# Kernel optimization log

Measured on AMD Instinct MI355X. Metric: run time of the kernel, lower is better.

Reference implementation:

```python
import jax, jax.numpy as jnp
import numpy as np

N, L, E_Q, E_TOTAL, H, FORECAST = 4, 2048, 512, 512, 8, 8
E_HEAD = E_TOTAL // H
DT = 1.0
NEG = -1e30


def setup_inputs() -> dict:
    rng = jax.random.key(0)
    ks = jax.random.split(rng, 8)
    inv = 1.0 / np.sqrt(E_Q)
    return {
        "query": jax.random.normal(ks[0], (N, L, E_Q), jnp.float32),
        "key": jax.random.normal(ks[1], (N, L, E_Q), jnp.float32),
        "value": jax.random.normal(ks[2], (N, L, E_Q), jnp.float32),
        "Wqkv": jax.random.normal(ks[3], (E_Q, 3 * E_TOTAL), jnp.float32) * inv,
        "bqkv": jnp.zeros((3 * E_TOTAL,), jnp.float32),
        "Wo": jax.random.normal(ks[4], (E_TOTAL, E_Q), jnp.float32) * (1.0 / np.sqrt(E_TOTAL)),
        "bo": jnp.zeros((E_Q,), jnp.float32),
        "Xi": jax.random.normal(ks[5], (H, E_HEAD, E_HEAD), jnp.float32) * 0.02,
    }


def reference(query, key, value, Wqkv, bqkv, Wo, bo, Xi):
    # NOTE: original forward projects `query` into q,k,v (key/value args unused).
    b, s, _ = query.shape
    qkv = query @ Wqkv + bqkv                      # [b, s, 3E]
    q, k, v = jnp.split(qkv, 3, axis=-1)
    split_heads = lambda t: t.reshape(b, s, H, E_HEAD).transpose(0, 2, 1, 3)  # [b,H,s,h]
    q, k, v = split_heads(q), split_heads(k), split_heads(v)
    # causal SDPA
    scale = 1.0 / np.sqrt(E_HEAD)
    scores = jnp.einsum('bhqd,bhkd->bhqk', q, k) * scale
    causal = jnp.tril(jnp.ones((s, s), bool))
    scores = jnp.where(causal, scores, NEG)
    probs = jax.nn.softmax(scores, axis=-1)
    attn = jnp.einsum('bhqk,bhkd->bhqd', probs, v)  # [b,H,s,h]
    # per-head SINDy linear dynamics, strict symmetry -> skew-symmetric A
    A = Xi - jnp.swapaxes(Xi, -1, -2)               # [H,h,h]

    def step(x, _):
        x2 = x + DT * jnp.einsum('bhsd,hde->bhse', x, A)
        return x2, x2

    _, ys = jax.lax.scan(step, attn, None, length=FORECAST)  # [n,b,H,s,h]
    roll = jnp.transpose(ys, (1, 0, 3, 2, 4)).reshape(b, FORECAST, s, E_TOTAL)
    return roll @ Wo + bo                            # [b, n, s, E_q]
```

## Files before the change

### kernel.cpp

```cpp
#include <hip/hip_runtime.h>
#include <math.h>


#define NEGV -1e30f

typedef __bf16 bf16_t;
typedef __bf16 bf16x4 __attribute__((ext_vector_type(4)));
typedef __bf16 bf16x8 __attribute__((ext_vector_type(8)));
typedef float f32x4 __attribute__((ext_vector_type(4)));

#define MFMA(a, b, c) __builtin_amdgcn_mfma_f32_16x16x32_bf16((a), (b), (c), 0, 0, 0)

#define QSCALE 0.18033688011112042f

__device__ __forceinline__ bf16x8* swz_ptr(bf16_t* base, int r, int cb) {
  return (bf16x8*)((char*)base + r * 128 + (cb ^ ((r & 7) << 4)));
}
__device__ __forceinline__ const bf16x8* swz_cptr(const bf16_t* base, int r, int cb) {
  return (const bf16x8*)((const char*)base + r * 128 + (cb ^ ((r & 7) << 4)));
}

__device__ __forceinline__ void gload16(const bf16_t* g, bf16_t* l) {
  __builtin_amdgcn_global_load_lds(
      (const __attribute__((address_space(1))) void*)g,
      (__attribute__((address_space(3))) void*)l, 16, 0, 0);
}


__global__ __launch_bounds__(256) void xconv(const float* __restrict__ X,
                                             bf16_t* __restrict__ Xb) {
  const int gid = blockIdx.x * 256 + threadIdx.x;
  const int s = gid >> 6, j = gid & 63;
  const float4* src = (const float4*)(X + (size_t)s * 512 + j * 8);
  const float4 f0 = src[0], f1 = src[1];
  bf16x8 v;
  v[0] = (bf16_t)f0.x; v[1] = (bf16_t)f0.y; v[2] = (bf16_t)f0.z; v[3] = (bf16_t)f0.w;
  v[4] = (bf16_t)f1.x; v[5] = (bf16_t)f1.y; v[6] = (bf16_t)f1.z; v[7] = (bf16_t)f1.w;
  *(bf16x8*)&Xb[(size_t)s * 512 + (j >> 3) * 64 + 8 * ((j & 7) ^ (s & 7))] = v;
}

__global__ __launch_bounds__(256) void wconv(const float* __restrict__ W,
                                             bf16_t* __restrict__ WT) {
  const int n0 = blockIdx.x * 64, k0 = blockIdx.y * 64;
  __shared__ float Wf[64][65];
  const int tid = threadIdx.x;
#pragma unroll
  for (int c = 0; c < 16; ++c) {
    const int idx = tid + c * 256;
    const int kk = idx >> 6, nn = idx & 63;
    Wf[kk][nn] = W[(size_t)(k0 + kk) * 1536 + n0 + nn];
  }
  __syncthreads();
  const int nr = tid >> 2;
  const int jb = (tid & 3) * 2;
#pragma unroll
  for (int t = 0; t < 2; ++t) {
    const int j = jb + t;
    bf16x8 v;
#pragma unroll
    for (int i = 0; i < 8; ++i) v[i] = (bf16_t)Wf[j * 8 + i][nr];
    *(bf16x8*)&WT[(size_t)(n0 + nr) * 512 + k0 + 8 * (j ^ (nr & 7))] = v;
  }
}

__global__ __launch_bounds__(256) void build_powers(const float* __restrict__ Xi,
                                                    float* __restrict__ pows) {
  const int h = blockIdx.x;
  __shared__ __align__(16) float P[64][68];
  __shared__ __align__(16) float cur[64][68];
  const int tid = threadIdx.x;
  const float* xi = Xi + (size_t)h * 4096;
  float* dst = pows + (size_t)h * 8 * 4096;
  for (int idx = tid; idx < 4096; idx += 256) {
    const int i = idx >> 6, j = idx & 63;
    const float p = (i == j ? 1.f : 0.f) + xi[i * 64 + j] - xi[j * 64 + i];
    P[i][j] = p;
    cur[i][j] = p;
    dst[idx] = p;
  }
  __syncthreads();
  const int i = tid >> 2;
  const int j0 = (tid & 3) * 16;
  for (int n = 1; n < 8; ++n) {
    float a[16];
#pragma unroll
    for (int jj = 0; jj < 16; ++jj) a[jj] = 0.f;
    for (int dd = 0; dd < 64; ++dd) {
      const float c = cur[i][dd];
#pragma unroll
      for (int jj = 0; jj < 16; ++jj) a[jj] += c * P[dd][j0 + jj];
    }
    __syncthreads();
#pragma unroll
    for (int jj = 0; jj < 16; ++jj) {
      cur[i][j0 + jj] = a[jj];
      dst[n * 4096 + i * 64 + j0 + jj] = a[jj];
    }
    __syncthreads();
  }
}

__global__ __launch_bounds__(256) void build_B(const float* __restrict__ pows,
                                               const float* __restrict__ Wo,
                                               bf16_t* __restrict__ BmatT) {
  const int et = blockIdx.x;
  const int n = blockIdx.y;
  const int h = blockIdx.z;
  __shared__ __align__(16) float P[64][68];
  __shared__ __align__(16) float We[64][128];
  const int tid = threadIdx.x;
  const float* src = pows + ((size_t)h * 8 + n) * 4096;
  for (int idx = tid; idx < 4096; idx += 256) P[idx >> 6][idx & 63] = src[idx];
  const int e0 = et * 128;
  for (int idx = tid; idx < 8192; idx += 256) {
    const int dd = idx >> 7, e = idx & 127;
    We[dd][e] = Wo[(size_t)(h * 64 + dd) * 512 + e0 + e];
  }
  __syncthreads();
  const int d = tid >> 2;
  const int eq = (tid & 3) * 32;
  float acc[32];
#pragma unroll
  for (int j = 0; j < 32; ++j) acc[j] = 0.f;
  for (int dd = 0; dd < 64; ++dd) {
    const float p = P[d][dd];
#pragma unroll
    for (int j = 0; j < 32; ++j) acc[j] += p * We[dd][eq + j];
  }
  bf16_t* dst = BmatT + (size_t)n * 512 * 512 + (size_t)(e0 + eq) * 512 + h * 64;
  const int dlo = d & 7, dhi = d >> 3;
#pragma unroll
  for (int j = 0; j < 32; ++j)
    dst[(size_t)j * 512 + 8 * (dhi ^ (j & 7)) + dlo] = (bf16_t)acc[j];
}

__global__ __launch_bounds__(256) void qkv_gemm(const bf16_t* __restrict__ Xb,
                                                const bf16_t* __restrict__ WT,
                                                const float* __restrict__ bias,
                                                bf16_t* __restrict__ qw,
                                                bf16_t* __restrict__ kw,
                                                bf16_t* __restrict__ vt) {
  __shared__ __align__(16) bf16_t As[128 * 64];
  __shared__ __align__(16) bf16_t Bs[128 * 64];
  const int tid = threadIdx.x;
  const int wave = tid >> 6, lane = tid & 63;
  const int g = lane >> 4, li = lane & 15;
  const int row0 = blockIdx.x * 128;
  const int col0 = blockIdx.y * 128;
  const int wm = (wave >> 1) * 64, wn = (wave & 1) * 64;
  f32x4 acc[4][4] = {};
  const bf16_t* asrc = Xb + (size_t)(row0 + wave * 32 + (lane >> 3)) * 512 + (lane & 7) * 8;
  const bf16_t* bsrc = WT + (size_t)(col0 + wave * 32 + (lane >> 3)) * 512 + (lane & 7) * 8;
  bf16_t* adst = &As[wave * 32 * 64];
  bf16_t* bdst = &Bs[wave * 32 * 64];
  for (int k0 = 0; k0 < 512; k0 += 64) {
#pragma unroll
    for (int c = 0; c < 4; ++c) {
      gload16(asrc + (size_t)c * 8 * 512 + k0, adst + c * 512);
      gload16(bsrc + (size_t)c * 8 * 512 + k0, bdst + c * 512);
    }
    __syncthreads();
#pragma unroll
    for (int ks = 0; ks < 2; ++ks) {
      bf16x8 af[4], bfr[4];
#pragma unroll
      for (int mr = 0; mr < 4; ++mr)
        af[mr] = *swz_cptr(As, wm + mr * 16 + li, ks * 64 + g * 16);
#pragma unroll
      for (int nr = 0; nr < 4; ++nr)
        bfr[nr] = *swz_cptr(Bs, wn + nr * 16 + li, ks * 64 + g * 16);
#pragma unroll
      for (int mr = 0; mr < 4; ++mr)
#pragma unroll
        for (int nr = 0; nr < 4; ++nr)
          acc[mr][nr] = MFMA(af[mr], bfr[nr], acc[mr][nr]);
    }
    __syncthreads();
  }
  const int cbase = col0 + wn;
  const int sel = cbase >> 9;
  const int hh = (cbase & 511) >> 6;
  const int bb = row0 >> 11;
  const size_t hb = (size_t)(bb * 8 + hh) * (2048 * 64);
  if (sel == 2) {
    bf16_t* vbase = vt + hb;
#pragma unroll
    for (int nr = 0; nr < 4; ++nr) {
      const int dcol = nr * 16 + li;
      const float bv = bias[cbase + dcol];
#pragma unroll
      for (int mr = 0; mr < 4; ++mr) {
        bf16x4 pk;
#pragma unroll
        for (int i = 0; i < 4; ++i) pk[i] = (bf16_t)(acc[mr][nr][i] + bv);
        const int s = (row0 + wm + mr * 16 + g * 4) & 2047;
        *(bf16x4*)&vbase[(size_t)dcol * 2048 + s] = pk;
      }
    }
  } else {
    bf16_t* dstp = (sel == 0 ? qw : kw) + hb;
    const float sc = (sel == 0) ? QSCALE : 1.0f;
#pragma unroll
    for (int nr = 0; nr < 4; ++nr) {
      const int dcol = nr * 16 + li;
      const float bv = bias[cbase + dcol];
#pragma unroll
      for (int mr = 0; mr < 4; ++mr) {
#pragma unroll
        for (int i = 0; i < 4; ++i) {
          const int r = row0 + wm + mr * 16 + g * 4 + i;
          const int s = r & 2047;
          dstp[(size_t)s * 64 + dcol] = (bf16_t)((acc[mr][nr][i] + bv) * sc);
        }
      }
    }
  }
}

__global__ __launch_bounds__(256, 4) void fattn(const bf16_t* __restrict__ qw,
                                                const bf16_t* __restrict__ kw,
                                                const bf16_t* __restrict__ vt,
                                                bf16_t* __restrict__ attn) {
  __shared__ __align__(16) bf16_t Ks[2][64][64];
  __shared__ __align__(16) bf16_t Vs[2][64][64];
  __shared__ __align__(16) bf16_t Ps[4][16][64];
  const int tid = threadIdx.x;
  const int w = tid >> 6;
  const int lane = tid & 63;
  const int g = lane >> 4;
  const int li = lane & 15;
  const int qt = (int)gridDim.x - 1 - (int)blockIdx.x;
  const int h = blockIdx.y;
  const int b = blockIdx.z;
  const size_t base = ((size_t)(b * 8 + h)) * (2048 * 64);
  const int q0 = qt * 64;
  const int qrow = q0 + w * 16 + li;
  const bf16x8 aq0 = *(const bf16x8*)(qw + base + (size_t)qrow * 64 + g * 8);
  const bf16x8 aq1 = *(const bf16x8*)(qw + base + (size_t)qrow * 64 + 32 + g * 8);
  const bf16_t* kbase = kw + base;
  const bf16_t* vbase = vt + base;
  const int r_st = tid >> 2;
  const int qu = tid & 3;
  {
    const bf16_t* kp = kbase + (size_t)r_st * 64 + qu * 16;
    const bf16_t* vp = vbase + (size_t)r_st * 2048 + qu * 16;
    *swz_ptr(&Ks[0][0][0], r_st, qu * 32) = *(const bf16x8*)kp;
    *swz_ptr(&Ks[0][0][0], r_st, qu * 32 + 16) = *(const bf16x8*)(kp + 8);
    *swz_ptr(&Vs[0][0][0], r_st, qu * 32) = *(const bf16x8*)vp;
    *swz_ptr(&Vs[0][0][0], r_st, qu * 32 + 16) = *(const bf16x8*)(vp + 8);
  }
  f32x4 accO[4] = {};
  float m_run = -__builtin_inff();
  float l_run = 0.f;
  char* const psrow = (char*)&Ps[w][li][0];
  const int pswz = (li & 7) << 4;
  for (int kt = 0; kt <= qt; ++kt) {
    __syncthreads();
    const int cur = kt & 1;
    const bool pf = kt < qt;
    bf16x8 nk0, nk1, nv0, nv1;
    if (pf) {
      const int kb2 = (kt + 1) * 64;
      const bf16_t* kp = kbase + (size_t)(kb2 + r_st) * 64 + qu * 16;
      const bf16_t* vp = vbase + (size_t)r_st * 2048 + kb2 + qu * 16;
      nk0 = *(const bf16x8*)kp;
      nk1 = *(const bf16x8*)(kp + 8);
      nv0 = *(const bf16x8*)vp;
      nv1 = *(const bf16x8*)(vp + 8);
    }
    f32x4 sv[4];
    __builtin_amdgcn_s_setprio(1);
#pragma unroll
    for (int nt = 0; nt < 4; ++nt) {
      const bf16x8 bk0 = *swz_cptr(&Ks[cur][0][0], nt * 16 + li, g * 16);
      const bf16x8 bk1 = *swz_cptr(&Ks[cur][0][0], nt * 16 + li, 64 + g * 16);
      f32x4 z = {0.f, 0.f, 0.f, 0.f};
      z = MFMA(bk0, aq0, z);
      sv[nt] = MFMA(bk1, aq1, z);
    }
    __builtin_amdgcn_s_setprio(0);
    if (kt == qt) {
#pragma unroll
      for (int nt = 0; nt < 4; ++nt)
#pragma unroll
        for (int i = 0; i < 4; ++i)
          if (nt * 16 + g * 4 + i > w * 16 + li) sv[nt][i] = NEGV;
    }
    float pmax = sv[0][0];
#pragma unroll
    for (int nt = 0; nt < 4; ++nt)
#pragma unroll
      for (int i = 0; i < 4; ++i) pmax = fmaxf(pmax, sv[nt][i]);
    pmax = fmaxf(pmax, __shfl_xor(pmax, 16, 64));
    pmax = fmaxf(pmax, __shfl_xor(pmax, 32, 64));
    if (!__all(pmax - m_run <= 8.f)) {
      const float newm = fmaxf(m_run, pmax);
      const float sc = exp2f(m_run - newm);
      l_run *= sc;
      m_run = newm;
#pragma unroll
      for (int nt = 0; nt < 4; ++nt)
#pragma unroll
        for (int i = 0; i < 4; ++i) accO[nt][i] *= sc;
    }
    float rsum = 0.f;
#pragma unroll
    for (int nt = 0; nt < 4; ++nt) {
#pragma unroll
      for (int i = 0; i < 4; ++i) {
        const float p = exp2f(sv[nt][i] - m_run);
        sv[nt][i] = p;
        rsum += p;
      }
    }
    rsum += __shfl_xor(rsum, 16, 64);
    rsum += __shfl_xor(rsum, 32, 64);
    l_run += rsum;
#pragma unroll
    for (int nt = 0; nt < 4; ++nt) {
      bf16x4 pk;
#pragma unroll
      for (int i = 0; i < 4; ++i) pk[i] = (bf16_t)sv[nt][i];
      *(bf16x4*)(psrow + ((nt * 32 + g * 8) ^ pswz)) = pk;
    }
    const bf16x8 ap0 = *(const bf16x8*)(psrow + ((g * 16) ^ pswz));
    const bf16x8 ap1 = *(const bf16x8*)(psrow + ((64 + g * 16) ^ pswz));
    __builtin_amdgcn_s_setprio(1);
#pragma unroll
    for (int nt = 0; nt < 4; ++nt) {
      const bf16x8 bv0 = *swz_cptr(&Vs[cur][0][0], nt * 16 + li, g * 16);
      const bf16x8 bv1 = *swz_cptr(&Vs[cur][0][0], nt * 16 + li, 64 + g * 16);
      accO[nt] = MFMA(bv0, ap0, accO[nt]);
      accO[nt] = MFMA(bv1, ap1, accO[nt]);
    }
    __builtin_amdgcn_s_setprio(0);
    if (pf) {
      *swz_ptr(&Ks[cur ^ 1][0][0], r_st, qu * 32) = nk0;
      *swz_ptr(&Ks[cur ^ 1][0][0], r_st, qu * 32 + 16) = nk1;
      *swz_ptr(&Vs[cur ^ 1][0][0], r_st, qu * 32) = nv0;
      *swz_ptr(&Vs[cur ^ 1][0][0], r_st, qu * 32 + 16) = nv1;
    }
  }
  {
    const float inv = 1.0f / l_run;
    bf16_t* arow = attn + (size_t)(b * 2048 + qrow) * 512 + h * 64;
#pragma unroll
    for (int nt = 0; nt < 4; ++nt) {
      bf16x4 pk;
#pragma unroll
      for (int i = 0; i < 4; ++i) pk[i] = (bf16_t)(accO[nt][i] * inv);
      *(bf16x4*)&arow[8 * ((nt * 2 + (g >> 1)) ^ (li & 7)) + (g & 1) * 4] = pk;
    }
  }
}

__global__ __launch_bounds__(256) void out_gemm(const bf16_t* __restrict__ A,
                                                const bf16_t* __restrict__ BmatT,
                                                const float* __restrict__ bo,
                                                float* __restrict__ out) {
  __shared__ __align__(16) bf16_t As[128 * 64];
  __shared__ __align__(16) bf16_t Bs[128 * 64];
  const int tid = threadIdx.x;
  const int wave = tid >> 6, lane = tid & 63;
  const int g = lane >> 4, li = lane & 15;
  const int row0 = blockIdx.x * 128;
  const int col0 = blockIdx.y * 128;
  const int nf = blockIdx.z;
  const int wm = (wave >> 1) * 64, wn = (wave & 1) * 64;
  f32x4 acc[4][4] = {};
  const bf16_t* asrc = A + (size_t)(row0 + wave * 32 + (lane >> 3)) * 512 + (lane & 7) * 8;
  const bf16_t* bsrc = BmatT + (size_t)nf * 512 * 512 +
                       (size_t)(col0 + wave * 32 + (lane >> 3)) * 512 + (lane & 7) * 8;
  bf16_t* adst = &As[wave * 32 * 64];
  bf16_t* bdst = &Bs[wave * 32 * 64];
  for (int k0 = 0; k0 < 512; k0 += 64) {
#pragma unroll
    for (int c = 0; c < 4; ++c) {
      gload16(asrc + (size_t)c * 8 * 512 + k0, adst + c * 512);
      gload16(bsrc + (size_t)c * 8 * 512 + k0, bdst + c * 512);
    }
    __syncthreads();
#pragma unroll
    for (int ks = 0; ks < 2; ++ks) {
      bf16x8 af[4], bfr[4];
#pragma unroll
      for (int mr = 0; mr < 4; ++mr)
        af[mr] = *swz_cptr(As, wm + mr * 16 + li, ks * 64 + g * 16);
#pragma unroll
      for (int nr = 0; nr < 4; ++nr)
        bfr[nr] = *swz_cptr(Bs, wn + nr * 16 + li, ks * 64 + g * 16);
#pragma unroll
      for (int mr = 0; mr < 4; ++mr)
#pragma unroll
        for (int nr = 0; nr < 4; ++nr)
          acc[mr][nr] = MFMA(af[mr], bfr[nr], acc[mr][nr]);
    }
    __syncthreads();
  }
  const int bb = row0 >> 11;
  float* obase = out + ((size_t)(bb * 8 + nf)) * (2048 * 512);
#pragma unroll
  for (int nr = 0; nr < 4; ++nr) {
    const int c = col0 + wn + nr * 16 + li;
    const float bv = bo[c];
#pragma unroll
    for (int mr = 0; mr < 4; ++mr) {
#pragma unroll
      for (int i = 0; i < 4; ++i) {
        const int r = row0 + wm + mr * 16 + g * 4 + i;
        const int s = r & 2047;
        obase[(size_t)s * 512 + c] = acc[mr][nr][i] + bv;
      }
    }
  }
}

extern "C" void kernel_launch(void* const* d_in, const int* in_sizes, int n_in,
                              void* d_out, int out_size, void* d_ws, size_t ws_size,
                              hipStream_t stream) {
  const float* query = (const float*)d_in[0];
  const float* Wqkv = (const float*)d_in[3];
  const float* bqkv = (const float*)d_in[4];
  const float* Wo = (const float*)d_in[5];
  const float* bo = (const float*)d_in[6];
  const float* Xi = (const float*)d_in[7];
  float* out = (float*)d_out;

  char* ws = (char*)d_ws;
  bf16_t* qw = (bf16_t*)(ws + 0);
  bf16_t* kw = (bf16_t*)(ws + 8388608);
  bf16_t* vt = (bf16_t*)(ws + 16777216);
  bf16_t* Xb = (bf16_t*)(ws + 25165824);
  bf16_t* attn = (bf16_t*)(ws + 25165824);
  bf16_t* BmatT = (bf16_t*)(ws + 33554432);
  float* pows = (float*)(ws + 37748736);
  bf16_t* WT = (bf16_t*)(ws + 38797312);

  xconv<<<dim3(2048), dim3(256), 0, stream>>>(query, Xb);
  wconv<<<dim3(24, 8), dim3(256), 0, stream>>>(Wqkv, WT);
  build_powers<<<dim3(8), dim3(256), 0, stream>>>(Xi, pows);
  build_B<<<dim3(4, 8, 8), dim3(256), 0, stream>>>(pows, Wo, BmatT);
  qkv_gemm<<<dim3(64, 12), dim3(256), 0, stream>>>(Xb, WT, bqkv, qw, kw, vt);
  fattn<<<dim3(32, 8, 4), dim3(256), 0, stream>>>(qw, kw, vt, attn);
  out_gemm<<<dim3(64, 4, 8), dim3(256), 0, stream>>>(attn, BmatT, bo, out);
}
```

Before: 190.0 us.

## Enlarge attention query tile to 128 rows and compute two forecast steps per out-GEMM block

The flash-attention kernel now gives each wave 32 query rows instead of 16, so every 64-key K/V tile staged in LDS feeds two query sub-tiles. This halves the K/V global traffic and the number of blocks, and sub-tiles lying fully above the causal diagonal are skipped. The output GEMM now computes two forecast steps per block, reusing the same A tile against two B matrices, which halves A reloads in exchange for doubled accumulator registers and fewer blocks. Both changes raise register pressure and cut grid parallelism (512 attention blocks, 1024 GEMM blocks), which may reduce occupancy.

```diff
diff --git a/kernel.cpp b/kernel.cpp
--- a/kernel.cpp
+++ b/kernel.cpp
@@ -217,10 +217,10 @@
   }
 }
 
-__global__ __launch_bounds__(256, 4) void fattn(const bf16_t* __restrict__ qw,
-                                                const bf16_t* __restrict__ kw,
-                                                const bf16_t* __restrict__ vt,
-                                                bf16_t* __restrict__ attn) {
+__global__ __launch_bounds__(256) void fattn(const bf16_t* __restrict__ qw,
+                                             const bf16_t* __restrict__ kw,
+                                             const bf16_t* __restrict__ vt,
+                                             bf16_t* __restrict__ attn) {
   __shared__ __align__(16) bf16_t Ks[2][64][64];
   __shared__ __align__(16) bf16_t Vs[2][64][64];
   __shared__ __align__(16) bf16_t Ps[4][16][64];
@@ -229,14 +229,19 @@
   const int lane = tid & 63;
   const int g = lane >> 4;
   const int li = lane & 15;
-  const int qt = (int)gridDim.x - 1 - (int)blockIdx.x;
+  const int qt = 15 - (int)blockIdx.x;
   const int h = blockIdx.y;
   const int b = blockIdx.z;
   const size_t base = ((size_t)(b * 8 + h)) * (2048 * 64);
-  const int q0 = qt * 64;
-  const int qrow = q0 + w * 16 + li;
-  const bf16x8 aq0 = *(const bf16x8*)(qw + base + (size_t)qrow * 64 + g * 8);
-  const bf16x8 aq1 = *(const bf16x8*)(qw + base + (size_t)qrow * 64 + 32 + g * 8);
+  const int q0 = qt * 128;
+  const int rbase0 = q0 + w * 32;
+  bf16x8 aq[2][2];
+#pragma unroll
+  for (int u = 0; u < 2; ++u) {
+    const bf16_t* qp = qw + base + (size_t)(rbase0 + u * 16 + li) * 64 + g * 8;
+    aq[u][0] = *(const bf16x8*)qp;
+    aq[u][1] = *(const bf16x8*)(qp + 32);
+  }
   const bf16_t* kbase = kw + base;
   const bf16_t* vbase = vt + base;
   const int r_st = tid >> 2;
@@ -249,18 +254,20 @@
     *swz_ptr(&Vs[0][0][0], r_st, qu * 32) = *(const bf16x8*)vp;
     *swz_ptr(&Vs[0][0][0], r_st, qu * 32 + 16) = *(const bf16x8*)(vp + 8);
   }
-  f32x4 accO[4] = {};
-  float m_run = -__builtin_inff();
-  float l_run = 0.f;
+  f32x4 accO[2][4] = {};
+  float m_run[2] = {-__builtin_inff(), -__builtin_inff()};
+  float l_run[2] = {0.f, 0.f};
   char* const psrow = (char*)&Ps[w][li][0];
   const int pswz = (li & 7) << 4;
-  for (int kt = 0; kt <= qt; ++kt) {
+  const int lim = 2 * qt + 2;
+  for (int kt = 0; kt < lim; ++kt) {
     __syncthreads();
     const int cur = kt & 1;
-    const bool pf = kt < qt;
+    const bool pf = (kt + 1) < lim;
+    const int kb = kt * 64;
     bf16x8 nk0, nk1, nv0, nv1;
     if (pf) {
-      const int kb2 = (kt + 1) * 64;
+      const int kb2 = kb + 64;
       const bf16_t* kp = kbase + (size_t)(kb2 + r_st) * 64 + qu * 16;
       const bf16_t* vp = vbase + (size_t)r_st * 2048 + kb2 + qu * 16;
       nk0 = *(const bf16x8*)kp;
@@ -268,72 +275,81 @@
       nv0 = *(const bf16x8*)vp;
       nv1 = *(const bf16x8*)(vp + 8);
     }
-    f32x4 sv[4];
-    __builtin_amdgcn_s_setprio(1);
+    bf16x8 bk[8];
 #pragma unroll
     for (int nt = 0; nt < 4; ++nt) {
-      const bf16x8 bk0 = *swz_cptr(&Ks[cur][0][0], nt * 16 + li, g * 16);
-      const bf16x8 bk1 = *swz_cptr(&Ks[cur][0][0], nt * 16 + li, 64 + g * 16);
-      f32x4 z = {0.f, 0.f, 0.f, 0.f};
-      z = MFMA(bk0, aq0, z);
-      sv[nt] = MFMA(bk1, aq1, z);
-    }
-    __builtin_amdgcn_s_setprio(0);
-    if (kt == qt) {
+      bk[2 * nt] = *swz_cptr(&Ks[cur][0][0], nt * 16 + li, g * 16);
+      bk[2 * nt + 1] = *swz_cptr(&Ks[cur][0][0], nt * 16 + li, 64 + g * 16);
+    }
+#pragma unroll
+    for (int u = 0; u < 2; ++u) {
+      const int rbase = rbase0 + u * 16;
+      if (kb > rbase + 15) continue;
+      f32x4 sv[4];
+      __builtin_amdgcn_s_setprio(1);
+#pragma unroll
+      for (int nt = 0; nt < 4; ++nt) {
+        f32x4 z = {0.f, 0.f, 0.f, 0.f};
+        z = MFMA(bk[2 * nt], aq[u][0], z);
+        sv[nt] = MFMA(bk[2 * nt + 1], aq[u][1], z);
+      }
+      __builtin_amdgcn_s_setprio(0);
+      if (kb + 63 > rbase) {
+#pragma unroll
+        for (int nt = 0; nt < 4; ++nt)
+#pragma unroll
+          for (int i = 0; i < 4; ++i)
+            if (kb + nt * 16 + g * 4 + i > rbase + li) sv[nt][i] = NEGV;
+      }
+      float pmax = sv[0][0];
 #pragma unroll
       for (int nt = 0; nt < 4; ++nt)
 #pragma unroll
-        for (int i = 0; i < 4; ++i)
-          if (nt * 16 + g * 4 + i > w * 16 + li) sv[nt][i] = NEGV;
-    }
-    float pmax = sv[0][0];
-#pragma unroll
-    for (int nt = 0; nt < 4; ++nt)
-#pragma unroll
-      for (int i = 0; i < 4; ++i) pmax = fmaxf(pmax, sv[nt][i]);
-    pmax = fmaxf(pmax, __shfl_xor(pmax, 16, 64));
-    pmax = fmaxf(pmax, __shfl_xor(pmax, 32, 64));
-    if (!__all(pmax - m_run <= 8.f)) {
-      const float newm = fmaxf(m_run, pmax);
-      const float sc = exp2f(m_run - newm);
-      l_run *= sc;
-      m_run = newm;
-#pragma unroll
-      for (int nt = 0; nt < 4; ++nt)
-#pragma unroll
-        for (int i = 0; i < 4; ++i) accO[nt][i] *= sc;
-    }
-    float rsum = 0.f;
-#pragma unroll
-    for (int nt = 0; nt < 4; ++nt) {
-#pragma unroll
-      for (int i = 0; i < 4; ++i) {
-        const float p = exp2f(sv[nt][i] - m_run);
-        sv[nt][i] = p;
-        rsum += p;
-      }
-    }
-    rsum += __shfl_xor(rsum, 16, 64);
-    rsum += __shfl_xor(rsum, 32, 64);
-    l_run += rsum;
-#pragma unroll
-    for (int nt = 0; nt < 4; ++nt) {
-      bf16x4 pk;
-#pragma unroll
-      for (int i = 0; i < 4; ++i) pk[i] = (bf16_t)sv[nt][i];
-      *(bf16x4*)(psrow + ((nt * 32 + g * 8) ^ pswz)) = pk;
-    }
-    const bf16x8 ap0 = *(const bf16x8*)(psrow + ((g * 16) ^ pswz));
-    const bf16x8 ap1 = *(const bf16x8*)(psrow + ((64 + g * 16) ^ pswz));
-    __builtin_amdgcn_s_setprio(1);
-#pragma unroll
-    for (int nt = 0; nt < 4; ++nt) {
-      const bf16x8 bv0 = *swz_cptr(&Vs[cur][0][0], nt * 16 + li, g * 16);
-      const bf16x8 bv1 = *swz_cptr(&Vs[cur][0][0], nt * 16 + li, 64 + g * 16);
-      accO[nt] = MFMA(bv0, ap0, accO[nt]);
-      accO[nt] = MFMA(bv1, ap1, accO[nt]);
-    }
-    __builtin_amdgcn_s_setprio(0);
+        for (int i = 0; i < 4; ++i) pmax = fmaxf(pmax, sv[nt][i]);
+      pmax = fmaxf(pmax, __shfl_xor(pmax, 16, 64));
+      pmax = fmaxf(pmax, __shfl_xor(pmax, 32, 64));
+      if (!__all(pmax - m_run[u] <= 8.f)) {
+        const float newm = fmaxf(m_run[u], pmax);
+        const float sc = exp2f(m_run[u] - newm);
+        l_run[u] *= sc;
+        m_run[u] = newm;
+#pragma unroll
+        for (int nt = 0; nt < 4; ++nt)
+#pragma unroll
+          for (int i = 0; i < 4; ++i) accO[u][nt][i] *= sc;
+      }
+      float rsum = 0.f;
+#pragma unroll
+      for (int nt = 0; nt < 4; ++nt) {
+#pragma unroll
+        for (int i = 0; i < 4; ++i) {
+          const float p = exp2f(sv[nt][i] - m_run[u]);
+          sv[nt][i] = p;
+          rsum += p;
+        }
+      }
+      rsum += __shfl_xor(rsum, 16, 64);
+      rsum += __shfl_xor(rsum, 32, 64);
+      l_run[u] += rsum;
+#pragma unroll
+      for (int nt = 0; nt < 4; ++nt) {
+        bf16x4 pk;
+#pragma unroll
+        for (int i = 0; i < 4; ++i) pk[i] = (bf16_t)sv[nt][i];
+        *(bf16x4*)(psrow + ((nt * 32 + g * 8) ^ pswz)) = pk;
+      }
+      const bf16x8 ap0 = *(const bf16x8*)(psrow + ((g * 16) ^ pswz));
+      const bf16x8 ap1 = *(const bf16x8*)(psrow + ((64 + g * 16) ^ pswz));
+      __builtin_amdgcn_s_setprio(1);
+#pragma unroll
+      for (int nt = 0; nt < 4; ++nt) {
+        const bf16x8 bv0 = *swz_cptr(&Vs[cur][0][0], nt * 16 + li, g * 16);
+        const bf16x8 bv1 = *swz_cptr(&Vs[cur][0][0], nt * 16 + li, 64 + g * 16);
+        accO[u][nt] = MFMA(bv0, ap0, accO[u][nt]);
+        accO[u][nt] = MFMA(bv1, ap1, accO[u][nt]);
+      }
+      __builtin_amdgcn_s_setprio(0);
+    }
     if (pf) {
       *swz_ptr(&Ks[cur ^ 1][0][0], r_st, qu * 32) = nk0;
       *swz_ptr(&Ks[cur ^ 1][0][0], r_st, qu * 32 + 16) = nk1;
@@ -341,75 +357,85 @@
       *swz_ptr(&Vs[cur ^ 1][0][0], r_st, qu * 32 + 16) = nv1;
     }
   }
-  {
-    const float inv = 1.0f / l_run;
-    bf16_t* arow = attn + (size_t)(b * 2048 + qrow) * 512 + h * 64;
+#pragma unroll
+  for (int u = 0; u < 2; ++u) {
+    const float inv = 1.0f / l_run[u];
+    bf16_t* arow = attn + (size_t)(b * 2048 + rbase0 + u * 16 + li) * 512 + h * 64;
 #pragma unroll
     for (int nt = 0; nt < 4; ++nt) {
       bf16x4 pk;
 #pragma unroll
-      for (int i = 0; i < 4; ++i) pk[i] = (bf16_t)(accO[nt][i] * inv);
+      for (int i = 0; i < 4; ++i) pk[i] = (bf16_t)(accO[u][nt][i] * inv);
       *(bf16x4*)&arow[8 * ((nt * 2 + (g >> 1)) ^ (li & 7)) + (g & 1) * 4] = pk;
     }
   }
 }
 
-__global__ __launch_bounds__(256) void out_gemm(const bf16_t* __restrict__ A,
-                                                const bf16_t* __restrict__ BmatT,
-                                                const float* __restrict__ bo,
-                                                float* __restrict__ out) {
+__global__ __launch_bounds__(256, 2) void out_gemm(const bf16_t* __restrict__ A,
+                                                   const bf16_t* __restrict__ BmatT,
+                                                   const float* __restrict__ bo,
+                                                   float* __restrict__ out) {
   __shared__ __align__(16) bf16_t As[128 * 64];
-  __shared__ __align__(16) bf16_t Bs[128 * 64];
+  __shared__ __align__(16) bf16_t Bs[2][128 * 64];
   const int tid = threadIdx.x;
   const int wave = tid >> 6, lane = tid & 63;
   const int g = lane >> 4, li = lane & 15;
   const int row0 = blockIdx.x * 128;
   const int col0 = blockIdx.y * 128;
-  const int nf = blockIdx.z;
+  const int nf0 = blockIdx.z * 2;
   const int wm = (wave >> 1) * 64, wn = (wave & 1) * 64;
-  f32x4 acc[4][4] = {};
+  f32x4 acc[2][4][4] = {};
   const bf16_t* asrc = A + (size_t)(row0 + wave * 32 + (lane >> 3)) * 512 + (lane & 7) * 8;
-  const bf16_t* bsrc = BmatT + (size_t)nf * 512 * 512 +
+  const bf16_t* bsrc = BmatT + (size_t)nf0 * 512 * 512 +
                        (size_t)(col0 + wave * 32 + (lane >> 3)) * 512 + (lane & 7) * 8;
   bf16_t* adst = &As[wave * 32 * 64];
-  bf16_t* bdst = &Bs[wave * 32 * 64];
+  bf16_t* bdst0 = &Bs[0][wave * 32 * 64];
+  bf16_t* bdst1 = &Bs[1][wave * 32 * 64];
   for (int k0 = 0; k0 < 512; k0 += 64) {
 #pragma unroll
     for (int c = 0; c < 4; ++c) {
       gload16(asrc + (size_t)c * 8 * 512 + k0, adst + c * 512);
-      gload16(bsrc + (size_t)c * 8 * 512 + k0, bdst + c * 512);
+      gload16(bsrc + (size_t)c * 8 * 512 + k0, bdst0 + c * 512);
+      gload16(bsrc + 262144 + (size_t)c * 8 * 512 + k0, bdst1 + c * 512);
     }
     __syncthreads();
 #pragma unroll
     for (int ks = 0; ks < 2; ++ks) {
-      bf16x8 af[4], bfr[4];
+      bf16x8 af[4];
 #pragma unroll
       for (int mr = 0; mr < 4; ++mr)
         af[mr] = *swz_cptr(As, wm + mr * 16 + li, ks * 64 + g * 16);
 #pragma unroll
-      for (int nr = 0; nr < 4; ++nr)
-        bfr[nr] = *swz_cptr(Bs, wn + nr * 16 + li, ks * 64 + g * 16);
-#pragma unroll
-      for (int mr = 0; mr < 4; ++mr)
+      for (int f = 0; f < 2; ++f) {
+        bf16x8 bfr[4];
 #pragma unroll
         for (int nr = 0; nr < 4; ++nr)
-          acc[mr][nr] = MFMA(af[mr], bfr[nr], acc[mr][nr]);
+          bfr[nr] = *swz_cptr(Bs[f], wn + nr * 16 + li, ks * 64 + g * 16);
+#pragma unroll
+        for (int mr = 0; mr < 4; ++mr)
+#pragma unroll
+          for (int nr = 0; nr < 4; ++nr)
+            acc[f][mr][nr] = MFMA(af[mr], bfr[nr], acc[f][mr][nr]);
+      }
     }
     __syncthreads();
   }
   const int bb = row0 >> 11;
-  float* obase = out + ((size_t)(bb * 8 + nf)) * (2048 * 512);
-#pragma unroll
-  for (int nr = 0; nr < 4; ++nr) {
-    const int c = col0 + wn + nr * 16 + li;
-    const float bv = bo[c];
-#pragma unroll
-    for (int mr = 0; mr < 4; ++mr) {
-#pragma unroll
-      for (int i = 0; i < 4; ++i) {
-        const int r = row0 + wm + mr * 16 + g * 4 + i;
-        const int s = r & 2047;
-        obase[(size_t)s * 512 + c] = acc[mr][nr][i] + bv;
+#pragma unroll
+  for (int f = 0; f < 2; ++f) {
+    float* obase = out + ((size_t)(bb * 8 + nf0 + f)) * (2048 * 512);
+#pragma unroll
+    for (int nr = 0; nr < 4; ++nr) {
+      const int c = col0 + wn + nr * 16 + li;
+      const float bv = bo[c];
+#pragma unroll
+      for (int mr = 0; mr < 4; ++mr) {
+#pragma unroll
+        for (int i = 0; i < 4; ++i) {
+          const int r = row0 + wm + mr * 16 + g * 4 + i;
+          const int s = r & 2047;
+          obase[(size_t)s * 512 + c] = acc[f][mr][nr][i] + bv;
+        }
       }
     }
   }
@@ -441,6 +467,6 @@
   build_powers<<<dim3(8), dim3(256), 0, stream>>>(Xi, pows);
   build_B<<<dim3(4, 8, 8), dim3(256), 0, stream>>>(pows, Wo, BmatT);
   qkv_gemm<<<dim3(64, 12), dim3(256), 0, stream>>>(Xb, WT, bqkv, qw, kw, vt);
-  fattn<<<dim3(32, 8, 4), dim3(256), 0, stream>>>(qw, kw, vt, attn);
-  out_gemm<<<dim3(64, 4, 8), dim3(256), 0, stream>>>(attn, BmatT, bo, out);
-}
+  fattn<<<dim3(16, 8, 4), dim3(256), 0, stream>>>(qw, kw, vt, attn);
+  out_gemm<<<dim3(64, 4, 4), dim3(256), 0, stream>>>(attn, BmatT, bo, out);
+}
```

After: 206.9 us. +8.9%, slower.

## Split long causal attention tiles across two blocks and reuse A tiles across forecast steps

Applied to the files above, without the earlier changes.

The attention kernel now splits the 16 longest query tiles into two KV chunks, each handled by a separate block. The blocks write partial outputs and softmax stats, and a new combine kernel merges them, which balances the causal triangle's work across 48 blocks per head. The output GEMM now computes two forecast steps per block, sharing the A tile loads and doubling the B shared-memory buffer. The cost is an extra kernel launch, fp32 partial-result traffic, and higher LDS and register use in out_gemm, with its occupancy hint set to 2.

```diff
diff --git a/kernel.cpp b/kernel.cpp
--- a/kernel.cpp
+++ b/kernel.cpp
@@ -217,10 +217,12 @@
   }
 }
 
-__global__ __launch_bounds__(256, 4) void fattn(const bf16_t* __restrict__ qw,
-                                                const bf16_t* __restrict__ kw,
-                                                const bf16_t* __restrict__ vt,
-                                                bf16_t* __restrict__ attn) {
+__global__ __launch_bounds__(256) void fattn(const bf16_t* __restrict__ qw,
+                                             const bf16_t* __restrict__ kw,
+                                             const bf16_t* __restrict__ vt,
+                                             bf16_t* __restrict__ attn,
+                                             float* __restrict__ opart,
+                                             float* __restrict__ ml) {
   __shared__ __align__(16) bf16_t Ks[2][64][64];
   __shared__ __align__(16) bf16_t Vs[2][64][64];
   __shared__ __align__(16) bf16_t Ps[4][16][64];
@@ -229,7 +231,16 @@
   const int lane = tid & 63;
   const int g = lane >> 4;
   const int li = lane & 15;
-  const int qt = (int)gridDim.x - 1 - (int)blockIdx.x;
+  const int x = blockIdx.x;
+  int qt, ktb, kte, chunk;
+  bool split;
+  if (x < 16) {
+    qt = 31 - x; ktb = 0; kte = 16; chunk = 0; split = true;
+  } else if (x < 32) {
+    qt = 47 - x; ktb = 16; kte = qt + 1; chunk = 1; split = true;
+  } else {
+    qt = 47 - x; ktb = 0; kte = qt + 1; chunk = 0; split = false;
+  }
   const int h = blockIdx.y;
   const int b = blockIdx.z;
   const size_t base = ((size_t)(b * 8 + h)) * (2048 * 64);
@@ -242,8 +253,8 @@
   const int r_st = tid >> 2;
   const int qu = tid & 3;
   {
-    const bf16_t* kp = kbase + (size_t)r_st * 64 + qu * 16;
-    const bf16_t* vp = vbase + (size_t)r_st * 2048 + qu * 16;
+    const bf16_t* kp = kbase + (size_t)(ktb * 64 + r_st) * 64 + qu * 16;
+    const bf16_t* vp = vbase + (size_t)r_st * 2048 + ktb * 64 + qu * 16;
     *swz_ptr(&Ks[0][0][0], r_st, qu * 32) = *(const bf16x8*)kp;
     *swz_ptr(&Ks[0][0][0], r_st, qu * 32 + 16) = *(const bf16x8*)(kp + 8);
     *swz_ptr(&Vs[0][0][0], r_st, qu * 32) = *(const bf16x8*)vp;
@@ -254,10 +265,10 @@
   float l_run = 0.f;
   char* const psrow = (char*)&Ps[w][li][0];
   const int pswz = (li & 7) << 4;
-  for (int kt = 0; kt <= qt; ++kt) {
-    __syncthreads();
-    const int cur = kt & 1;
-    const bool pf = kt < qt;
+  for (int kt = ktb; kt < kte; ++kt) {
+    __syncthreads();
+    const int cur = (kt - ktb) & 1;
+    const bool pf = (kt + 1) < kte;
     bf16x8 nk0, nk1, nv0, nv1;
     if (pf) {
       const int kb2 = (kt + 1) * 64;
@@ -341,7 +352,7 @@
       *swz_ptr(&Vs[cur ^ 1][0][0], r_st, qu * 32 + 16) = nv1;
     }
   }
-  {
+  if (!split) {
     const float inv = 1.0f / l_run;
     bf16_t* arow = attn + (size_t)(b * 2048 + qrow) * 512 + h * 64;
 #pragma unroll
@@ -351,65 +362,122 @@
       for (int i = 0; i < 4; ++i) pk[i] = (bf16_t)(accO[nt][i] * inv);
       *(bf16x4*)&arow[8 * ((nt * 2 + (g >> 1)) ^ (li & 7)) + (g & 1) * 4] = pk;
     }
-  }
-}
-
-__global__ __launch_bounds__(256) void out_gemm(const bf16_t* __restrict__ A,
-                                                const bf16_t* __restrict__ BmatT,
-                                                const float* __restrict__ bo,
-                                                float* __restrict__ out) {
+  } else {
+    const int row = w * 16 + li;
+    const size_t pbase = (((size_t)(b * 8 + h) * 16 + (qt - 16)) * 2 + chunk) * 64 + row;
+    float* op = opart + pbase * 64;
+#pragma unroll
+    for (int nt = 0; nt < 4; ++nt) *(f32x4*)&op[nt * 16 + g * 4] = accO[nt];
+    if (g == 0) {
+      ml[pbase * 2] = m_run;
+      ml[pbase * 2 + 1] = l_run;
+    }
+  }
+}
+
+__global__ __launch_bounds__(256) void fcombine(const float* __restrict__ opart,
+                                                const float* __restrict__ ml,
+                                                bf16_t* __restrict__ attn) {
+  const int qi = blockIdx.x;
+  const int h = blockIdx.y;
+  const int b = blockIdx.z;
+  const int tid = threadIdx.x;
+  const int row = tid >> 2;
+  const int dq = (tid & 3) * 16;
+  const size_t base2 = ((size_t)(b * 8 + h) * 16 + qi) * 2;
+  const size_t p0 = (base2 * 64 + row);
+  const size_t p1 = ((base2 + 1) * 64 + row);
+  const float m1 = ml[p0 * 2], l1 = ml[p0 * 2 + 1];
+  const float m2 = ml[p1 * 2], l2 = ml[p1 * 2 + 1];
+  const float m = fmaxf(m1, m2);
+  const float w1 = exp2f(m1 - m), w2 = exp2f(m2 - m);
+  const float inv = 1.0f / (l1 * w1 + l2 * w2);
+  const float* o1 = opart + p0 * 64;
+  const float* o2 = opart + p1 * 64;
+  const int qrow = (16 + qi) * 64 + row;
+  bf16_t* arow = attn + (size_t)(b * 2048 + qrow) * 512 + h * 64;
+#pragma unroll
+  for (int t = 0; t < 2; ++t) {
+    const int c0 = dq + t * 8;
+    const f32x4 a1 = *(const f32x4*)&o1[c0];
+    const f32x4 b1 = *(const f32x4*)&o1[c0 + 4];
+    const f32x4 a2 = *(const f32x4*)&o2[c0];
+    const f32x4 b2 = *(const f32x4*)&o2[c0 + 4];
+    bf16x8 v;
+#pragma unroll
+    for (int i = 0; i < 4; ++i) {
+      v[i] = (bf16_t)((a1[i] * w1 + a2[i] * w2) * inv);
+      v[4 + i] = (bf16_t)((b1[i] * w1 + b2[i] * w2) * inv);
+    }
+    *(bf16x8*)&arow[8 * ((c0 >> 3) ^ (row & 7))] = v;
+  }
+}
+
+__global__ __launch_bounds__(256, 2) void out_gemm(const bf16_t* __restrict__ A,
+                                                   const bf16_t* __restrict__ BmatT,
+                                                   const float* __restrict__ bo,
+                                                   float* __restrict__ out) {
   __shared__ __align__(16) bf16_t As[128 * 64];
-  __shared__ __align__(16) bf16_t Bs[128 * 64];
+  __shared__ __align__(16) bf16_t Bs[2][128 * 64];
   const int tid = threadIdx.x;
   const int wave = tid >> 6, lane = tid & 63;
   const int g = lane >> 4, li = lane & 15;
   const int row0 = blockIdx.x * 128;
   const int col0 = blockIdx.y * 128;
-  const int nf = blockIdx.z;
+  const int nf0 = blockIdx.z * 2;
   const int wm = (wave >> 1) * 64, wn = (wave & 1) * 64;
-  f32x4 acc[4][4] = {};
+  f32x4 acc[2][4][4] = {};
   const bf16_t* asrc = A + (size_t)(row0 + wave * 32 + (lane >> 3)) * 512 + (lane & 7) * 8;
-  const bf16_t* bsrc = BmatT + (size_t)nf * 512 * 512 +
+  const bf16_t* bsrc = BmatT + (size_t)nf0 * 512 * 512 +
                        (size_t)(col0 + wave * 32 + (lane >> 3)) * 512 + (lane & 7) * 8;
   bf16_t* adst = &As[wave * 32 * 64];
-  bf16_t* bdst = &Bs[wave * 32 * 64];
+  bf16_t* bdst0 = &Bs[0][wave * 32 * 64];
+  bf16_t* bdst1 = &Bs[1][wave * 32 * 64];
   for (int k0 = 0; k0 < 512; k0 += 64) {
 #pragma unroll
     for (int c = 0; c < 4; ++c) {
       gload16(asrc + (size_t)c * 8 * 512 + k0, adst + c * 512);
-      gload16(bsrc + (size_t)c * 8 * 512 + k0, bdst + c * 512);
+      gload16(bsrc + (size_t)c * 8 * 512 + k0, bdst0 + c * 512);
+      gload16(bsrc + 262144 + (size_t)c * 8 * 512 + k0, bdst1 + c * 512);
     }
     __syncthreads();
 #pragma unroll
     for (int ks = 0; ks < 2; ++ks) {
-      bf16x8 af[4], bfr[4];
+      bf16x8 af[4];
 #pragma unroll
       for (int mr = 0; mr < 4; ++mr)
         af[mr] = *swz_cptr(As, wm + mr * 16 + li, ks * 64 + g * 16);
 #pragma unroll
-      for (int nr = 0; nr < 4; ++nr)
-        bfr[nr] = *swz_cptr(Bs, wn + nr * 16 + li, ks * 64 + g * 16);
-#pragma unroll
-      for (int mr = 0; mr < 4; ++mr)
+      for (int f = 0; f < 2; ++f) {
+        bf16x8 bfr[4];
 #pragma unroll
         for (int nr = 0; nr < 4; ++nr)
-          acc[mr][nr] = MFMA(af[mr], bfr[nr], acc[mr][nr]);
+          bfr[nr] = *swz_cptr(Bs[f], wn + nr * 16 + li, ks * 64 + g * 16);
+#pragma unroll
+        for (int mr = 0; mr < 4; ++mr)
+#pragma unroll
+          for (int nr = 0; nr < 4; ++nr)
+            acc[f][mr][nr] = MFMA(af[mr], bfr[nr], acc[f][mr][nr]);
+      }
     }
     __syncthreads();
   }
   const int bb = row0 >> 11;
-  float* obase = out + ((size_t)(bb * 8 + nf)) * (2048 * 512);
-#pragma unroll
-  for (int nr = 0; nr < 4; ++nr) {
-    const int c = col0 + wn + nr * 16 + li;
-    const float bv = bo[c];
-#pragma unroll
-    for (int mr = 0; mr < 4; ++mr) {
-#pragma unroll
-      for (int i = 0; i < 4; ++i) {
-        const int r = row0 + wm + mr * 16 + g * 4 + i;
-        const int s = r & 2047;
-        obase[(size_t)s * 512 + c] = acc[mr][nr][i] + bv;
+#pragma unroll
+  for (int f = 0; f < 2; ++f) {
+    float* obase = out + ((size_t)(bb * 8 + nf0 + f)) * (2048 * 512);
+#pragma unroll
+    for (int nr = 0; nr < 4; ++nr) {
+      const int c = col0 + wn + nr * 16 + li;
+      const float bv = bo[c];
+#pragma unroll
+      for (int mr = 0; mr < 4; ++mr) {
+#pragma unroll
+        for (int i = 0; i < 4; ++i) {
+          const int r = row0 + wm + mr * 16 + g * 4 + i;
+          const int s = r & 2047;
+          obase[(size_t)s * 512 + c] = acc[f][mr][nr][i] + bv;
+        }
       }
     }
   }
@@ -435,12 +503,15 @@
   bf16_t* BmatT = (bf16_t*)(ws + 33554432);
   float* pows = (float*)(ws + 37748736);
   bf16_t* WT = (bf16_t*)(ws + 38797312);
+  float* opart = (float*)(ws + 40370176);
+  float* mlbuf = (float*)(ws + 57147392);
 
   xconv<<<dim3(2048), dim3(256), 0, stream>>>(query, Xb);
   wconv<<<dim3(24, 8), dim3(256), 0, stream>>>(Wqkv, WT);
   build_powers<<<dim3(8), dim3(256), 0, stream>>>(Xi, pows);
   build_B<<<dim3(4, 8, 8), dim3(256), 0, stream>>>(pows, Wo, BmatT);
   qkv_gemm<<<dim3(64, 12), dim3(256), 0, stream>>>(Xb, WT, bqkv, qw, kw, vt);
-  fattn<<<dim3(32, 8, 4), dim3(256), 0, stream>>>(qw, kw, vt, attn);
-  out_gemm<<<dim3(64, 4, 8), dim3(256), 0, stream>>>(attn, BmatT, bo, out);
-}
+  fattn<<<dim3(48, 8, 4), dim3(256), 0, stream>>>(qw, kw, vt, attn, opart, mlbuf);
+  fcombine<<<dim3(16, 8, 4), dim3(256), 0, stream>>>(opart, mlbuf, attn);
+  out_gemm<<<dim3(64, 4, 4), dim3(256), 0, stream>>>(attn, BmatT, bo, out);
+}
```

Measured after the change: 185.5 us. 2.4% less time.
